# Optimization experiments

Measured on AMD Instinct MI355X. Metric: run time of the kernel, lower is better.

The kernel has to match this reference:

```python
import jax, jax.numpy as jnp
import numpy as np

H = 256   # encoder/decoder hidden size
U = 128   # attention units


def setup_inputs() -> dict:
    key = jax.random.key(0)
    ks = jax.random.split(key, 8)
    B, Td, Te = 16, 128, 1024
    s = 1.0 / np.sqrt(H)
    return {
        "dec_outputs": jax.random.normal(ks[0], (B, Td, H), dtype=jnp.float32),
        "enc_outputs": jax.random.normal(ks[1], (B, Te, H), dtype=jnp.float32),
        "W1": jax.random.normal(ks[2], (H, U), dtype=jnp.float32) * s,
        "b1": jnp.zeros((U,), dtype=jnp.float32),
        "W2": jax.random.normal(ks[3], (H, U), dtype=jnp.float32) * s,
        "b2": jnp.zeros((U,), dtype=jnp.float32),
        "V": jax.random.normal(ks[4], (U, 1), dtype=jnp.float32) * (1.0 / np.sqrt(U)),
        "bv": jnp.zeros((1,), dtype=jnp.float32),
    }


def reference(dec_outputs, enc_outputs, W1, b1, W2, b2, V, bv):
    # Project once (the original redundantly re-projects enc_outputs per step).
    # w1d: [B, Td, U], w2e: [B, Te, U]
    w1d = jnp.einsum("bth,hu->btu", dec_outputs, W1) + b1
    w2e = jnp.einsum("bsh,hu->bsu", enc_outputs, W2) + b2
    # Additive Bahdanau score: tanh over broadcast sum -> [B, Td, Te, U]
    feat = jnp.tanh(w1d[:, :, None, :] + w2e[:, None, :, :])
    # V projection to scalar score: [B, Td, Te]
    score = jnp.einsum("btsu,u->bts", feat, V[:, 0]) + bv[0]
    # Softmax over encoder positions (original Softmax(axis=1) on [B, Te])
    return jax.nn.softmax(score, axis=-1)
```

## Files before the change

kernel.cpp:

```cpp
#include <hip/hip_runtime.h>
#include <math.h>

#define HB 256
#define UB 128
#define BB 16
#define TD 128
#define TE 1024

#define CLAMP_W 7.0f
#define L2E2 2.8853900817779268f
#define ALPHA 1.52587890625e-05f
#define NEG2ALPHA (-3.0517578125e-05f)

#define PINV(x) asm volatile("" : "+v"(x))
#define PINS(x) asm volatile("" : "+s"(x))
#define PINV4(q) do { PINV((q).x); PINV((q).y); PINV((q).z); PINV((q).w); } while (0)
#define PINS4(q) do { PINS((q).x); PINS((q).y); PINS((q).z); PINS((q).w); } while (0)

__device__ __forceinline__ float stage_exp(float w, float shift) {
    float t = fminf(fmaxf(w, -CLAMP_W), CLAMP_W);
    return exp2f(fmaf(t, L2E2, shift));
}

#define DEC_SLABS 32
#define NSLABS 288
#define PROJ_BLOCKS (NSLABS * 2)

__global__ __launch_bounds__(512) void proj_v12(
    const float* __restrict__ dec, const float* __restrict__ enc,
    const float* __restrict__ W1, const float* __restrict__ b1,
    const float* __restrict__ W2, const float* __restrict__ b2,
    float* __restrict__ Ea, float* __restrict__ Eb) {
    const int blk = blockIdx.x;
    const int slab = blk >> 1, uhalf = blk & 1;
    const bool is_dec = slab < DEC_SLABS;
    const int rel = is_dec ? slab : slab - DEC_SLABS;
    const float* __restrict__ X    = is_dec ? dec : enc;
    const float* __restrict__ W    = is_dec ? W1 : W2;
    const float* __restrict__ bias = is_dec ? b1 : b2;

    __shared__ float xt[HB][66];
    const int tid = threadIdx.x;
    const long row0 = (long)rel * 64;

    #pragma unroll
    for (int it = 0; it < 8; ++it) {
        int idx = it * 512 + tid;
        int row = idx >> 6, hf4 = idx & 63;
        float4 f = *reinterpret_cast<const float4*>(X + (row0 + row) * HB + hf4 * 4);
        xt[hf4 * 4 + 0][row] = f.x;
        xt[hf4 * 4 + 1][row] = f.y;
        xt[hf4 * 4 + 2][row] = f.z;
        xt[hf4 * 4 + 3][row] = f.w;
    }
    __syncthreads();

    const int l = tid & 63;
    const int w = __builtin_amdgcn_readfirstlane(tid >> 6);
    const int ub3 = w & 3;
    const int ub  = ub3 + uhalf * 4;
    const int hh  = w >> 2;
    const int u0  = ub * 16;
    const int h0  = hh * 128;

    float acc[16];
    #pragma unroll
    for (int j = 0; j < 16; ++j) acc[j] = 0.f;

    for (int h = 0; h < 128; h += 4) {
        const int hg = h0 + h;
        float4 wf[4][4];
        #pragma unroll
        for (int k = 0; k < 4; ++k)
            #pragma unroll
            for (int q = 0; q < 4; ++q)
                wf[k][q] = *reinterpret_cast<const float4*>(
                    W + (hg + k) * UB + u0 + q * 4);
        float xk[4];
        #pragma unroll
        for (int k = 0; k < 4; ++k) xk[k] = xt[hg + k][l];
        #pragma unroll
        for (int k = 0; k < 4; ++k)
            #pragma unroll
            for (int q = 0; q < 4; ++q) {
                acc[q * 4 + 0] = fmaf(xk[k], wf[k][q].x, acc[q * 4 + 0]);
                acc[q * 4 + 1] = fmaf(xk[k], wf[k][q].y, acc[q * 4 + 1]);
                acc[q * 4 + 2] = fmaf(xk[k], wf[k][q].z, acc[q * 4 + 2]);
                acc[q * 4 + 3] = fmaf(xk[k], wf[k][q].w, acc[q * 4 + 3]);
            }
    }

    __syncthreads();
    float4* red = reinterpret_cast<float4*>(&xt[0][0]);
    if (hh == 1) {
        #pragma unroll
        for (int q = 0; q < 4; ++q)
            red[((ub3 * 64 + l) << 2) + q] =
                make_float4(acc[q * 4], acc[q * 4 + 1], acc[q * 4 + 2], acc[q * 4 + 3]);
    }
    __syncthreads();
    if (hh == 0) {
        #pragma unroll
        for (int q = 0; q < 4; ++q) {
            float4 r = red[((ub3 * 64 + l) << 2) + q];
            acc[q * 4 + 0] += r.x; acc[q * 4 + 1] += r.y;
            acc[q * 4 + 2] += r.z; acc[q * 4 + 3] += r.w;
        }
        const float sh = is_dec ? -16.f : 0.f;
        const int POS  = is_dec ? TD : TE;
        const long bq  = row0 / POS;
        const int pos  = (int)(row0 % POS) + l;
        float4* dst4 = reinterpret_cast<float4*>(is_dec ? Ea : Eb);
        #pragma unroll
        for (int q = 0; q < 4; ++q) {
            float4 o = make_float4(
                stage_exp(acc[q * 4 + 0] + bias[u0 + q * 4 + 0], sh),
                stage_exp(acc[q * 4 + 1] + bias[u0 + q * 4 + 1], sh),
                stage_exp(acc[q * 4 + 2] + bias[u0 + q * 4 + 2], sh),
                stage_exp(acc[q * 4 + 3] + bias[u0 + q * 4 + 3], sh));
            dst4[(bq * 32 + ub * 4 + q) * (long)POS + pos] = o;
        }
    }
}

__global__ __launch_bounds__(512) void score_v9(
    const float* __restrict__ Ea4,
    const float4* __restrict__ Eb4,
    const float* __restrict__ V,
    float* __restrict__ outraw) {
    const int tid = threadIdx.x;
    const int i = blockIdx.x;
    const int xcd = i & 7, j = i >> 3;
    const int b     = 2 * xcd + (j >> 4);
    const int tgrp  = (j >> 1) & 7;
    const int shalf = j & 1;
    const int t0 = tgrp * 16;
    const int s  = shalf * 512 + tid;

    const float*  ab = Ea4 + ((long)b * 32 * TD + t0) * 4;
    const float4* ep = Eb4 + (long)b * 32 * TE + s;
    const float alphav = ALPHA;

    float acc[16];
    #pragma unroll
    for (int t = 0; t < 16; ++t) acc[t] = 0.f;

    float4 a[16], vC, vN, eC, eN;
    vC = *reinterpret_cast<const float4*>(V);
    eC = ep[0];

    for (int u4 = 0; u4 < 32; ++u4) {
        const int p = (u4 + 1 < 32) ? u4 + 1 : 0;
        eN = ep[(long)p * TE];
        vN = *reinterpret_cast<const float4*>(V + p * 4);
        const float* _a = ab + (long)u4 * (TD * 4);
        #pragma unroll
        for (int t = 0; t < 16; ++t)
            a[t] = *reinterpret_cast<const float4*>(_a + t * 4);
        PINS4(a[15]);
        #pragma unroll
        for (int t = 0; t < 16; ++t) {
            float4 A = a[t];
            float X0 = fmaf(A.x, eC.x, alphav);
            float X1 = fmaf(A.y, eC.y, alphav);
            float X2 = fmaf(A.z, eC.z, alphav);
            float X3 = fmaf(A.w, eC.w, alphav);
            float P01 = X0 * X1, P23 = X2 * X3;
            float N01 = fmaf(vC.x, X1, vC.y * X0);
            float N23 = fmaf(vC.z, X3, vC.w * X2);
            float N   = fmaf(N01, P23, N23 * P01);
            acc[t] = fmaf(N, __builtin_amdgcn_rcpf(P01 * P23), acc[t]);
        }
        PINV4(eN);
        PINS4(vN);
        eC = eN; vC = vN;
    }

    float* orow = outraw + ((long)b * TD + t0) * TE + s;
    #pragma unroll
    for (int t = 0; t < 16; ++t)
        orow[(long)t * TE] = NEG2ALPHA * acc[t];
}

__global__ __launch_bounds__(1024) void softmax_v9(float* __restrict__ out) {
    const long row = blockIdx.x;
    float* p = out + row * TE;
    const int tid = threadIdx.x;
    const int wv = tid >> 6, l = tid & 63;

    float x = p[tid];
    __shared__ float red[16];
    float m = x;
    #pragma unroll
    for (int off = 32; off > 0; off >>= 1) m = fmaxf(m, __shfl_xor(m, off, 64));
    if (l == 0) red[wv] = m;
    __syncthreads();
    #pragma unroll
    for (int k = 0; k < 16; ++k) m = fmaxf(m, red[k]);
    __syncthreads();
    float e = __expf(x - m);
    float si = e;
    #pragma unroll
    for (int off = 32; off > 0; off >>= 1) si += __shfl_xor(si, off, 64);
    if (l == 0) red[wv] = si;
    __syncthreads();
    si = 0.f;
    #pragma unroll
    for (int k = 0; k < 16; ++k) si += red[k];
    p[tid] = e * (1.f / si);
}

extern "C" void kernel_launch(void* const* d_in, const int* in_sizes, int n_in,
                              void* d_out, int out_size, void* d_ws, size_t ws_size,
                              hipStream_t stream) {
    const float* dec = (const float*)d_in[0];
    const float* enc = (const float*)d_in[1];
    const float* W1  = (const float*)d_in[2];
    const float* b1  = (const float*)d_in[3];
    const float* W2  = (const float*)d_in[4];
    const float* b2  = (const float*)d_in[5];
    const float* V   = (const float*)d_in[6];
    float* out = (float*)d_out;

    float* Ea = (float*)d_ws;
    float* Eb = Ea + (long)BB * 32 * TD * 4;

    proj_v12<<<PROJ_BLOCKS, 512, 0, stream>>>(dec, enc, W1, b1, W2, b2, Ea, Eb);
    score_v9<<<256, 512, 0, stream>>>(Ea, (const float4*)Eb, V, out);
    softmax_v9<<<BB * TD, 1024, 0, stream>>>(out);
}
```

Measured before the change: 67.86 us.

## Use packed FP32 math in score kernel with t-pair interleaved decoder layout

The decoder projection output Ea is rewritten in an interleaved layout where adjacent decoder positions sit next to each other for each unit. This lets the score kernel process two decoder rows at once with v_pk_fma_f32/v_pk_mul_f32 inline assembly, roughly halving VALU instruction count for the product-ratio evaluation. Decoder values now come in through vector-register loads through a pinned pointer instead of scalar loads, which costs more VGPRs and vector memory traffic. The reciprocals stay scalar, one per lane element.

```diff
diff --git a/kernel.cpp b/kernel.cpp
--- a/kernel.cpp
+++ b/kernel.cpp
@@ -12,10 +12,30 @@
 #define ALPHA 1.52587890625e-05f
 #define NEG2ALPHA (-3.0517578125e-05f)
 
+typedef __attribute__((ext_vector_type(2))) float f32x2;
+
 #define PINV(x) asm volatile("" : "+v"(x))
-#define PINS(x) asm volatile("" : "+s"(x))
 #define PINV4(q) do { PINV((q).x); PINV((q).y); PINV((q).z); PINV((q).w); } while (0)
-#define PINS4(q) do { PINS((q).x); PINS((q).y); PINS((q).z); PINS((q).w); } while (0)
+#define PINPTR(p) asm volatile("" : "+v"(p))
+
+#define PKOP3(name, MODS)                                                     \
+__device__ __forceinline__ f32x2 name(f32x2 a, f32x2 b, f32x2 c) {            \
+    f32x2 d;                                                                  \
+    asm("v_pk_fma_f32 %0, %1, %2, %3" MODS                                    \
+        : "=v"(d) : "v"(a), "v"(b), "v"(c));                                  \
+    return d;                                                                 \
+}
+#define PKOP2(name, MODS)                                                     \
+__device__ __forceinline__ f32x2 name(f32x2 a, f32x2 b) {                     \
+    f32x2 d;                                                                  \
+    asm("v_pk_mul_f32 %0, %1, %2" MODS : "=v"(d) : "v"(a), "v"(b));           \
+    return d;                                                                 \
+}
+PKOP3(pk_fma,     "")
+PKOP3(pk_fma_blo, " op_sel:[0,0,0] op_sel_hi:[1,0,1]")
+PKOP3(pk_fma_bhi, " op_sel:[0,1,0] op_sel_hi:[1,1,1]")
+PKOP2(pk_mul,     "")
+PKOP2(pk_mul_bhi, " op_sel:[0,1] op_sel_hi:[1,1]")
 
 __device__ __forceinline__ float stage_exp(float w, float shift) {
     float t = fminf(fmaxf(w, -CLAMP_W), CLAMP_W);
@@ -106,25 +126,35 @@
             acc[q * 4 + 0] += r.x; acc[q * 4 + 1] += r.y;
             acc[q * 4 + 2] += r.z; acc[q * 4 + 3] += r.w;
         }
-        const float sh = is_dec ? -16.f : 0.f;
-        const int POS  = is_dec ? TD : TE;
-        const long bq  = row0 / POS;
-        const int pos  = (int)(row0 % POS) + l;
-        float4* dst4 = reinterpret_cast<float4*>(is_dec ? Ea : Eb);
-        #pragma unroll
-        for (int q = 0; q < 4; ++q) {
-            float4 o = make_float4(
-                stage_exp(acc[q * 4 + 0] + bias[u0 + q * 4 + 0], sh),
-                stage_exp(acc[q * 4 + 1] + bias[u0 + q * 4 + 1], sh),
-                stage_exp(acc[q * 4 + 2] + bias[u0 + q * 4 + 2], sh),
-                stage_exp(acc[q * 4 + 3] + bias[u0 + q * 4 + 3], sh));
-            dst4[(bq * 32 + ub * 4 + q) * (long)POS + pos] = o;
+        if (is_dec) {
+            const long bq = row0 >> 7;
+            const int pos = (int)(row0 & 127) + l;
+            float* dp = Ea + (((bq * 32 + ub * 4) * 64L + (pos >> 1)) * 8) + (pos & 1);
+            #pragma unroll
+            for (int q = 0; q < 4; ++q)
+                #pragma unroll
+                for (int j2 = 0; j2 < 4; ++j2)
+                    dp[q * 512 + j2 * 2] =
+                        stage_exp(acc[q * 4 + j2] + bias[u0 + q * 4 + j2], -16.f);
+        } else {
+            const long bq = row0 >> 10;
+            const int pos = (int)(row0 & (TE - 1)) + l;
+            float4* dst4 = reinterpret_cast<float4*>(Eb);
+            #pragma unroll
+            for (int q = 0; q < 4; ++q) {
+                float4 o = make_float4(
+                    stage_exp(acc[q * 4 + 0] + bias[u0 + q * 4 + 0], 0.f),
+                    stage_exp(acc[q * 4 + 1] + bias[u0 + q * 4 + 1], 0.f),
+                    stage_exp(acc[q * 4 + 2] + bias[u0 + q * 4 + 2], 0.f),
+                    stage_exp(acc[q * 4 + 3] + bias[u0 + q * 4 + 3], 0.f));
+                dst4[(bq * 32 + ub * 4 + q) * (long)TE + pos] = o;
+            }
         }
     }
 }
 
-__global__ __launch_bounds__(512) void score_v9(
-    const float* __restrict__ Ea4,
+__global__ __launch_bounds__(512) void score_v14(
+    const float* __restrict__ Ea2,
     const float4* __restrict__ Eb4,
     const float* __restrict__ V,
     float* __restrict__ outraw) {
@@ -137,49 +167,55 @@
     const int t0 = tgrp * 16;
     const int s  = shalf * 512 + tid;
 
-    const float*  ab = Ea4 + ((long)b * 32 * TD + t0) * 4;
-    const float4* ep = Eb4 + (long)b * 32 * TE + s;
-    const float alphav = ALPHA;
-
-    float acc[16];
-    #pragma unroll
-    for (int t = 0; t < 16; ++t) acc[t] = 0.f;
-
-    float4 a[16], vC, vN, eC, eN;
-    vC = *reinterpret_cast<const float4*>(V);
-    eC = ep[0];
-
+    const float* ab = Ea2 + (long)b * 32 * 512 + (t0 >> 1) * 8;
+    const float* vb = V;
+    PINPTR(ab);
+    PINPTR(vb);
+    const float4* __restrict__ ep = Eb4 + (long)b * 32 * TE + s;
+
+    const f32x2 al2 = {ALPHA, ALPHA};
+    f32x2 acc2[8];
+    #pragma unroll
+    for (int tp = 0; tp < 8; ++tp) acc2[tp] = (f32x2){0.f, 0.f};
+
+    float4 eC = ep[0], eN;
     for (int u4 = 0; u4 < 32; ++u4) {
         const int p = (u4 + 1 < 32) ? u4 + 1 : 0;
         eN = ep[(long)p * TE];
-        vN = *reinterpret_cast<const float4*>(V + p * 4);
-        const float* _a = ab + (long)u4 * (TD * 4);
-        #pragma unroll
-        for (int t = 0; t < 16; ++t)
-            a[t] = *reinterpret_cast<const float4*>(_a + t * 4);
-        PINS4(a[15]);
-        #pragma unroll
-        for (int t = 0; t < 16; ++t) {
-            float4 A = a[t];
-            float X0 = fmaf(A.x, eC.x, alphav);
-            float X1 = fmaf(A.y, eC.y, alphav);
-            float X2 = fmaf(A.z, eC.z, alphav);
-            float X3 = fmaf(A.w, eC.w, alphav);
-            float P01 = X0 * X1, P23 = X2 * X3;
-            float N01 = fmaf(vC.x, X1, vC.y * X0);
-            float N23 = fmaf(vC.z, X3, vC.w * X2);
-            float N   = fmaf(N01, P23, N23 * P01);
-            acc[t] = fmaf(N, __builtin_amdgcn_rcpf(P01 * P23), acc[t]);
+        float4 vv = *reinterpret_cast<const float4*>(vb + u4 * 4);
+        f32x2 e01 = {eC.x, eC.y}, e23 = {eC.z, eC.w};
+        f32x2 v01 = {vv.x, vv.y}, v23 = {vv.z, vv.w};
+        const float* abase = ab + (long)u4 * 512;
+        #pragma unroll
+        for (int tp = 0; tp < 8; ++tp) {
+            float4 aA = *reinterpret_cast<const float4*>(abase + tp * 8);
+            float4 aB = *reinterpret_cast<const float4*>(abase + tp * 8 + 4);
+            f32x2 a0 = {aA.x, aA.y}, a1 = {aA.z, aA.w};
+            f32x2 a2 = {aB.x, aB.y}, a3 = {aB.z, aB.w};
+            f32x2 X0 = pk_fma_blo(a0, e01, al2);
+            f32x2 X1 = pk_fma_bhi(a1, e01, al2);
+            f32x2 X2 = pk_fma_blo(a2, e23, al2);
+            f32x2 X3 = pk_fma_bhi(a3, e23, al2);
+            f32x2 P01 = pk_mul(X0, X1), P23 = pk_mul(X2, X3);
+            f32x2 N01 = pk_fma_blo(X1, v01, pk_mul_bhi(X0, v01));
+            f32x2 N23 = pk_fma_blo(X3, v23, pk_mul_bhi(X2, v23));
+            f32x2 N   = pk_fma(N01, P23, pk_mul(N23, P01));
+            f32x2 P   = pk_mul(P01, P23);
+            float r0 = __builtin_amdgcn_rcpf(P.x);
+            float r1 = __builtin_amdgcn_rcpf(P.y);
+            acc2[tp].x = fmaf(N.x, r0, acc2[tp].x);
+            acc2[tp].y = fmaf(N.y, r1, acc2[tp].y);
         }
         PINV4(eN);
-        PINS4(vN);
-        eC = eN; vC = vN;
+        eC = eN;
     }
 
     float* orow = outraw + ((long)b * TD + t0) * TE + s;
     #pragma unroll
-    for (int t = 0; t < 16; ++t)
-        orow[(long)t * TE] = NEG2ALPHA * acc[t];
+    for (int tp = 0; tp < 8; ++tp) {
+        orow[(long)(2 * tp) * TE]     = NEG2ALPHA * acc2[tp].x;
+        orow[(long)(2 * tp + 1) * TE] = NEG2ALPHA * acc2[tp].y;
+    }
 }
 
 __global__ __launch_bounds__(1024) void softmax_v9(float* __restrict__ out) {
@@ -226,6 +262,6 @@
     float* Eb = Ea + (long)BB * 32 * TD * 4;
 
     proj_v12<<<PROJ_BLOCKS, 512, 0, stream>>>(dec, enc, W1, b1, W2, b2, Ea, Eb);
-    score_v9<<<256, 512, 0, stream>>>(Ea, (const float4*)Eb, V, out);
+    score_v14<<<256, 512, 0, stream>>>(Ea, (const float4*)Eb, V, out);
     softmax_v9<<<BB * TD, 1024, 0, stream>>>(out);
 }
```

New measurement: 80.81 us. +19.1%, slower.
